# Performance work log

Hardware: AMD Instinct MI355X
Metric: run time of the kernel (lower is better)

The kernel has to match this reference:

```python
import jax, jax.numpy as jnp
import numpy as np

N = 10000; E = 160000; NF = 5; EF = 3; H = 8; C = 128; HC = H * C; G = 16

def _glorot(key, shape):
    s = float(np.sqrt(6.0 / (shape[0] + shape[-1])))
    return jax.random.uniform(key, shape, minval=-s, maxval=s, dtype=jnp.float32)

def setup_inputs():
    key = jax.random.key(0)
    ks = jax.random.split(key, 32)
    inp = {}
    inp["x"] = jax.random.normal(ks[0], (N, NF), dtype=jnp.float32)
    inp["edge_index"] = jax.random.randint(ks[1], (2, E), 0, N, dtype=jnp.int32)
    inp["edge_attr"] = jax.random.normal(ks[2], (E, EF), dtype=jnp.float32)
    inp["batch"] = jnp.sort(jax.random.randint(ks[3], (N,), 0, G, dtype=jnp.int32))
    ins = [NF, HC, HC, HC]
    i = 4
    for l in range(4):
        inp[f"W{l+1}"] = _glorot(ks[i], (ins[l], HC)); i += 1
        inp[f"We{l+1}"] = _glorot(ks[i], (EF, HC)); i += 1
        inp[f"as{l+1}"] = _glorot(ks[i], (H, C)); i += 1
        inp[f"ad{l+1}"] = _glorot(ks[i], (H, C)); i += 1
        inp[f"ae{l+1}"] = _glorot(ks[i], (H, C)); i += 1
        inp[f"b{l+1}"] = jnp.zeros((HC if l < 3 else C,), jnp.float32)
    inp["lin_w"] = _glorot(ks[i], (C, 1)) * 2.0
    inp["lin_b"] = jnp.zeros((1,), jnp.float32)
    return inp

def _gat(x, src, dst, ea, W, We, a_s, a_d, a_e, bias, concat):
    # PyG GATConv with edge_dim, add_self_loops=True, fill_value='mean'
    n = x.shape[0]
    cnt = jax.ops.segment_sum(jnp.ones((src.shape[0],), x.dtype), dst, n)
    loop_attr = jax.ops.segment_sum(ea, dst, n) / jnp.maximum(cnt, 1.0)[:, None]
    sl = jnp.arange(n, dtype=src.dtype)
    src2 = jnp.concatenate([src, sl])
    dst2 = jnp.concatenate([dst, sl])
    ea2 = jnp.concatenate([ea, loop_attr], axis=0)
    xl = (x @ W).reshape(n, H, C)                       # [N,H,C]
    a_src = jnp.einsum("nhc,hc->nh", xl, a_s)
    a_dst = jnp.einsum("nhc,hc->nh", xl, a_d)
    el = (ea2 @ We).reshape(-1, H, C)                    # [E2,H,C]
    alpha = a_src[src2] + a_dst[dst2] + jnp.einsum("ehc,hc->eh", el, a_e)
    alpha = jax.nn.leaky_relu(alpha, 0.2)
    m = jax.ops.segment_max(alpha, dst2, n)
    m = jnp.where(jnp.isfinite(m), m, 0.0)
    ex = jnp.exp(alpha - m[dst2])
    den = jax.ops.segment_sum(ex, dst2, n)
    alpha = ex / (den[dst2] + 1e-16)                     # segment softmax over dst
    out = jax.ops.segment_sum(alpha[:, :, None] * xl[src2], dst2, n)  # [N,H,C]
    if concat:
        return out.reshape(n, HC) + bias
    return out.mean(axis=1) + bias

def reference(x, edge_index, edge_attr, batch,
              W1, We1, as1, ad1, ae1, b1,
              W2, We2, as2, ad2, ae2, b2,
              W3, We3, as3, ad3, ae3, b3,
              W4, We4, as4, ad4, ae4, b4,
              lin_w, lin_b):
    src, dst = edge_index[0], edge_index[1]
    h = jax.nn.elu(_gat(x, src, dst, edge_attr, W1, We1, as1, ad1, ae1, b1, True))
    h = jax.nn.elu(_gat(h, src, dst, edge_attr, W2, We2, as2, ad2, ae2, b2, True))
    h = jax.nn.elu(_gat(h, src, dst, edge_attr, W3, We3, as3, ad3, ae3, b3, True))
    h = jax.nn.elu(_gat(h, src, dst, edge_attr, W4, We4, as4, ad4, ae4, b4, False))
    cnt = jax.ops.segment_sum(jnp.ones((N,), h.dtype), batch, G)
    pooled = jax.ops.segment_sum(h, batch, G) / jnp.maximum(cnt, 1.0)[:, None]
    return (pooled @ lin_w + lin_b).squeeze(-1)
```

## Files before the change

kernel.cpp:

```cpp
#include <hip/hip_runtime.h>
#include <math.h>

#define Nn 10000
#define En 160000
#define NF 5
#define EF 3
#define Hh 8
#define Cc 128
#define HC 1024
#define Gg 16

#define Mpad 10112

typedef __attribute__((ext_vector_type(8))) _Float16 half8;
typedef __attribute__((ext_vector_type(4))) float f32x4;


__device__ __forceinline__ void gl_lds16(const void* g, void* l) {
    __builtin_amdgcn_global_load_lds((const __attribute__((address_space(1))) void*)g,
                                     (__attribute__((address_space(3))) void*)l, 16, 0, 0);
}

__device__ __forceinline__ float elu_f(float v) {
    return (v > 0.f) ? v : expm1f(v);
}


__global__ void deg_sum_k(const int* __restrict__ dst, int* __restrict__ cnt) {
    int e = blockIdx.x * 256 + threadIdx.x;
    if (e >= En) return;
    atomicAdd(&cnt[dst[e]], 1);
}

__global__ __launch_bounds__(1024) void scan_k(const int* __restrict__ cnt,
                                               int* __restrict__ rowptr,
                                               int* __restrict__ fillptr,
                                               const int* __restrict__ batch,
                                               int* __restrict__ gstart) {
    __shared__ int sh[1024];
    int tid = threadIdx.x;
    int base = tid * 10;
    int loc[10];
    int tsum = 0;
#pragma unroll
    for (int j = 0; j < 10; ++j) {
        int i = base + j;
        int v = (i < Nn) ? cnt[i] : 0;
        loc[j] = tsum;
        tsum += v;
    }
    sh[tid] = tsum;
    __syncthreads();
    for (int off = 1; off < 1024; off <<= 1) {
        int t = (tid >= off) ? sh[tid - off] : 0;
        __syncthreads();
        sh[tid] += t;
        __syncthreads();
    }
    int excl = sh[tid] - tsum;
#pragma unroll
    for (int j = 0; j < 10; ++j) {
        int i = base + j;
        if (i < Nn) {
            rowptr[i] = excl + loc[j];
            fillptr[i] = excl + loc[j];
        }
    }
    if (tid == 1023) rowptr[Nn] = sh[1023];
#pragma unroll
    for (int j = 0; j < 10; ++j) {
        int i = base + j;
        if (i < Nn) {
            int b = batch[i];
            if (i == 0) {
                for (int g = 0; g <= b; ++g) gstart[g] = 0;
            } else {
                int pb = batch[i - 1];
                for (int g = pb + 1; g <= b; ++g) gstart[g] = i;
            }
            if (i == Nn - 1) {
                for (int g = b + 1; g <= Gg; ++g) gstart[g] = Nn;
            }
        }
    }
}

__global__ void csr_fill_k(const int* __restrict__ src, const int* __restrict__ dst,
                           const float* __restrict__ ea, int* __restrict__ fillptr,
                           float4* __restrict__ eaP, float* __restrict__ loop_attr) {
    int e = blockIdx.x * 256 + threadIdx.x;
    if (e >= En) return;
    int d = dst[e];
    float e0 = ea[e * 3 + 0], e1 = ea[e * 3 + 1], e2 = ea[e * 3 + 2];
    int pos = atomicAdd(&fillptr[d], 1);
    eaP[pos] = make_float4(e0, e1, e2, __int_as_float(src[e]));
    atomicAdd(&loop_attr[d * 3 + 0], e0);
    atomicAdd(&loop_attr[d * 3 + 1], e1);
    atomicAdd(&loop_attr[d * 3 + 2], e2);
}


__global__ void wae_all_k(const float* __restrict__ We1, const float* __restrict__ ae1,
                          const float* __restrict__ We2, const float* __restrict__ ae2,
                          const float* __restrict__ We3, const float* __restrict__ ae3,
                          const float* __restrict__ We4, const float* __restrict__ ae4,
                          float* __restrict__ w_ae_all) {
    int t = threadIdx.x;
    if (t >= 96) return;
    int l = t / 24, idx = t % 24;
    int f = idx >> 3, h = idx & 7;
    const float* We = (l == 0) ? We1 : (l == 1) ? We2 : (l == 2) ? We3 : We4;
    const float* ae = (l == 0) ? ae1 : (l == 1) ? ae2 : (l == 2) ? ae3 : ae4;
    float s = 0.f;
    for (int c = 0; c < Cc; ++c) s += We[f * HC + h * Cc + c] * ae[h * Cc + c];
    w_ae_all[l * 24 + f * 8 + h] = s;
}

__global__ __launch_bounds__(1024) void wsplit_all_k(const float* __restrict__ W2,
                                                     const float* __restrict__ W3,
                                                     const float* __restrict__ W4,
                                                     _Float16* __restrict__ Wt16) {
    __shared__ float tile[32][33];
    int z = blockIdx.z;
    const float* W = (z == 0) ? W2 : (z == 1) ? W3 : W4;
    int nb = blockIdx.x * 32, kb = blockIdx.y * 32;
    tile[threadIdx.y][threadIdx.x] = W[(size_t)(kb + threadIdx.y) * HC + nb + threadIdx.x];
    __syncthreads();
    float x = tile[threadIdx.x][threadIdx.y];
    int n = nb + threadIdx.y, k = kb + threadIdx.x;
    Wt16[(size_t)z * HC * HC + (size_t)n * HC + k] = (_Float16)x;
}


__global__ void gemm_k5(const float* __restrict__ x, const float* __restrict__ Wm,
                        const float* __restrict__ a_s, const float* __restrict__ a_d,
                        _Float16* __restrict__ out16,
                        float* __restrict__ a_srcB, float* __restrict__ a_dstB) {
    int n = blockIdx.x;
    int tid = threadIdx.x;
    __shared__ float xr[8];
    __shared__ float vrow[HC];
    if (tid < NF) xr[tid] = x[n * NF + tid];
    __syncthreads();
    float x0 = xr[0], x1 = xr[1], x2 = xr[2], x3 = xr[3], x4 = xr[4];
    for (int j = tid; j < HC; j += 256) {
        float v = x0 * Wm[j] + x1 * Wm[HC + j] + x2 * Wm[2 * HC + j]
                + x3 * Wm[3 * HC + j] + x4 * Wm[4 * HC + j];
        out16[(size_t)n * HC + j] = (_Float16)v;
        vrow[j] = v;
    }
    __syncthreads();
    int w = tid >> 6, lane = tid & 63;
#pragma unroll
    for (int q = 0; q < 2; ++q) {
        int h = w * 2 + q;
        float v0 = vrow[h * Cc + lane], v1 = vrow[h * Cc + 64 + lane];
        float s1 = v0 * a_s[h * Cc + lane] + v1 * a_s[h * Cc + 64 + lane];
        float s2 = v0 * a_d[h * Cc + lane] + v1 * a_d[h * Cc + 64 + lane];
#pragma unroll
        for (int off = 32; off; off >>= 1) {
            s1 += __shfl_xor(s1, off);
            s2 += __shfl_xor(s2, off);
        }
        if (lane == 0) { a_srcB[n * 8 + h] = s1; a_dstB[n * 8 + h] = s2; }
    }
}

__global__ __launch_bounds__(256) void gemm_mfma(const _Float16* __restrict__ A,
                                                 const _Float16* __restrict__ Bt,
                                                 const float* __restrict__ a_s,
                                                 const float* __restrict__ a_d,
                                                 _Float16* __restrict__ C16,
                                                 float* __restrict__ a_srcB,
                                                 float* __restrict__ a_dstB) {
    __shared__ _Float16 As[128 * 32];
    __shared__ _Float16 Bs[128 * 32];
    __shared__ float ps[128][2];
    __shared__ float pd[128][2];
    int tid = threadIdx.x;
    int wave = tid >> 6, lane = tid & 63;
    int wr = wave >> 1, wc = wave & 1;
    int row0 = blockIdx.y * 128;
    int col0 = blockIdx.x * 128;
    int h = blockIdx.x;

    f32x4 acc[4][4];
#pragma unroll
    for (int i = 0; i < 4; ++i)
#pragma unroll
        for (int j = 0; j < 4; ++j) acc[i][j] = (f32x4){0.f, 0.f, 0.f, 0.f};

    int srow = lane >> 2;
    int scol = (lane & 3) * 8;
    int fr = lane & 15;
    int fk = (lane >> 4) * 8;

    for (int kb = 0; kb < 1024; kb += 32) {
#pragma unroll
        for (int cc = 0; cc < 2; ++cc) {
            int c = wave + cc * 4;
            int r = c * 16 + srow;
            gl_lds16(A + (size_t)(row0 + r) * 1024 + kb + scol, &As[c * 512 + lane * 8]);
            gl_lds16(Bt + (size_t)(col0 + r) * 1024 + kb + scol, &Bs[c * 512 + lane * 8]);
        }
        __syncthreads();

        half8 af[4], bf[4];
#pragma unroll
        for (int i = 0; i < 4; ++i)
            af[i] = *(const half8*)&As[(wr * 64 + i * 16 + fr) * 32 + fk];
#pragma unroll
        for (int j = 0; j < 4; ++j)
            bf[j] = *(const half8*)&Bs[(wc * 64 + j * 16 + fr) * 32 + fk];
#pragma unroll
        for (int i = 0; i < 4; ++i)
#pragma unroll
            for (int j = 0; j < 4; ++j)
                acc[i][j] = __builtin_amdgcn_mfma_f32_16x16x32_f16(af[i], bf[j], acc[i][j],
                                                                   0, 0, 0);
        __syncthreads();
    }

    int cn = lane & 15, rq = (lane >> 4) * 4;
#pragma unroll
    for (int i = 0; i < 4; ++i) {
        int rbase = row0 + wr * 64 + i * 16 + rq;
#pragma unroll
        for (int j = 0; j < 4; ++j) {
            int col = col0 + wc * 64 + j * 16 + cn;
#pragma unroll
            for (int r = 0; r < 4; ++r) {
                int row = rbase + r;
                if (row < Nn) C16[(size_t)row * HC + col] = (_Float16)acc[i][j][r];
            }
        }
    }
    float asv[4], adv[4];
#pragma unroll
    for (int j = 0; j < 4; ++j) {
        int c = wc * 64 + j * 16 + cn;
        asv[j] = a_s[h * Cc + c];
        adv[j] = a_d[h * Cc + c];
    }
#pragma unroll
    for (int i = 0; i < 4; ++i)
#pragma unroll
        for (int r = 0; r < 4; ++r) {
            float rs = acc[i][0][r] * asv[0] + acc[i][1][r] * asv[1]
                     + acc[i][2][r] * asv[2] + acc[i][3][r] * asv[3];
            float rd = acc[i][0][r] * adv[0] + acc[i][1][r] * adv[1]
                     + acc[i][2][r] * adv[2] + acc[i][3][r] * adv[3];
#pragma unroll
            for (int off = 1; off < 16; off <<= 1) {
                rs += __shfl_xor(rs, off);
                rd += __shfl_xor(rd, off);
            }
            if (cn == 0) {
                int rib = wr * 64 + i * 16 + rq + r;
                ps[rib][wc] = rs;
                pd[rib][wc] = rd;
            }
        }
    __syncthreads();
    if (tid < 128) {
        int row = row0 + tid;
        if (row < Nn) {
            a_srcB[row * 8 + h] = ps[tid][0] + ps[tid][1];
            a_dstB[row * 8 + h] = pd[tid][0] + pd[tid][1];
        }
    }
}


__global__ __launch_bounds__(256) void aggregate_k(const _Float16* __restrict__ xl16,
                                                   const float4* __restrict__ eaP,
                                                   const float* __restrict__ loop_attr,
                                                   const float* __restrict__ a_srcB,
                                                   const float* __restrict__ a_dstB,
                                                   const float* __restrict__ w_ae,
                                                   const int* __restrict__ rowptr,
                                                   const float* __restrict__ bias,
                                                   const float* __restrict__ lin_w,
                                                   _Float16* __restrict__ A2,
                                                   float* __restrict__ dnode,
                                                   int raw_mode) {
    __shared__ float cmbA[3][1024];
    __shared__ float cmbS[3][64];
    int sub = threadIdx.x >> 6;
    int lane = threadIdx.x & 63;
    int n = blockIdx.x;
    int beg = rowptr[n], end = rowptr[n + 1];
    int hc = lane >> 3;

    float w0c = w_ae[hc], w1c = w_ae[8 + hc], w2c = w_ae[16 + hc];
    float adst_n = a_dstB[n * 8 + hc];
    float asrc_n = a_srcB[n * 8 + hc];
    float invd = 1.0f / fmaxf((float)(end - beg), 1.0f);
    float f0 = loop_attr[n * 3 + 0] * invd;
    float f1 = loop_attr[n * 3 + 1] * invd;
    float f2 = loop_attr[n * 3 + 2] * invd;
    float av = asrc_n + adst_n + f0 * w0c + f1 * w1c + f2 * w2c;
    float aself = (av > 0.f) ? av : 0.2f * av;

    float acc[16];
    float s;
    int loff = lane * 16;
    if (sub == 0) {
        const _Float16* r = xl16 + (size_t)n * HC + loff;
        half8 r0 = *(const half8*)r;
        half8 r1 = *(const half8*)(r + 8);
#pragma unroll
        for (int j = 0; j < 8; ++j) {
            acc[j] = (float)r0[j];
            acc[8 + j] = (float)r1[j];
        }
        s = 1.0f;
    } else {
#pragma unroll
        for (int j = 0; j < 16; ++j) acc[j] = 0.f;
        s = 0.0f;
    }

    for (int i0 = beg + sub; i0 < end; i0 += 16) {
        bool v1 = (i0 + 4 < end), v2 = (i0 + 8 < end), v3 = (i0 + 12 < end);
        int i1 = v1 ? i0 + 4 : i0;
        int i2 = v2 ? i0 + 8 : i0;
        int i3 = v3 ? i0 + 12 : i0;
        float4 e0 = eaP[i0], e1 = eaP[i1], e2 = eaP[i2], e3 = eaP[i3];
        int s0 = __float_as_int(e0.w), s1 = __float_as_int(e1.w);
        int s2 = __float_as_int(e2.w), s3 = __float_as_int(e3.w);
        float as0 = a_srcB[s0 * 8 + hc], as1 = a_srcB[s1 * 8 + hc];
        float as2 = a_srcB[s2 * 8 + hc], as3 = a_srcB[s3 * 8 + hc];
        const _Float16* p0 = xl16 + (size_t)s0 * HC + loff;
        const _Float16* p1 = xl16 + (size_t)s1 * HC + loff;
        const _Float16* p2 = xl16 + (size_t)s2 * HC + loff;
        const _Float16* p3 = xl16 + (size_t)s3 * HC + loff;
        half8 q0a = *(const half8*)p0, q0b = *(const half8*)(p0 + 8);
        half8 q1a = *(const half8*)p1, q1b = *(const half8*)(p1 + 8);
        half8 q2a = *(const half8*)p2, q2b = *(const half8*)(p2 + 8);
        half8 q3a = *(const half8*)p3, q3b = *(const half8*)(p3 + 8);
        float al0 = as0 + adst_n + e0.x * w0c + e0.y * w1c + e0.z * w2c;
        float al1 = as1 + adst_n + e1.x * w0c + e1.y * w1c + e1.z * w2c;
        float al2 = as2 + adst_n + e2.x * w0c + e2.y * w1c + e2.z * w2c;
        float al3 = as3 + adst_n + e3.x * w0c + e3.y * w1c + e3.z * w2c;
        al0 = (al0 > 0.f) ? al0 : 0.2f * al0;
        al1 = (al1 > 0.f) ? al1 : 0.2f * al1;
        al2 = (al2 > 0.f) ? al2 : 0.2f * al2;
        al3 = (al3 > 0.f) ? al3 : 0.2f * al3;
        float u0 = __expf(al0 - aself);
        float u1 = v1 ? __expf(al1 - aself) : 0.f;
        float u2 = v2 ? __expf(al2 - aself) : 0.f;
        float u3 = v3 ? __expf(al3 - aself) : 0.f;
        s += u0 + u1 + u2 + u3;
#pragma unroll
        for (int j = 0; j < 8; ++j) {
            float t0 = acc[j], t1 = acc[8 + j];
            t0 = fmaf(u0, (float)q0a[j], t0);  t1 = fmaf(u0, (float)q0b[j], t1);
            t0 = fmaf(u1, (float)q1a[j], t0);  t1 = fmaf(u1, (float)q1b[j], t1);
            t0 = fmaf(u2, (float)q2a[j], t0);  t1 = fmaf(u2, (float)q2b[j], t1);
            t0 = fmaf(u3, (float)q3a[j], t0);  t1 = fmaf(u3, (float)q3b[j], t1);
            acc[j] = t0; acc[8 + j] = t1;
        }
    }

    if (sub != 0) {
#pragma unroll
        for (int j = 0; j < 4; ++j)
            *(float4*)&cmbA[sub - 1][loff + j * 4] = *(const float4*)&acc[j * 4];
        cmbS[sub - 1][lane] = s;
    }
    __syncthreads();
    if (sub != 0) return;

#pragma unroll
    for (int k = 0; k < 3; ++k) {
        s += cmbS[k][lane];
#pragma unroll
        for (int j = 0; j < 4; ++j) {
            float4 c4 = *(const float4*)&cmbA[k][loff + j * 4];
            acc[j * 4 + 0] += c4.x;
            acc[j * 4 + 1] += c4.y;
            acc[j * 4 + 2] += c4.z;
            acc[j * 4 + 3] += c4.w;
        }
    }
    float inv = 1.f / (s + 1e-16f);

    if (!raw_mode) {
        int ch = loff;
        half8 hv0, hv1;
#pragma unroll
        for (int j = 0; j < 8; ++j) {
            hv0[j] = (_Float16)elu_f(fmaf(acc[j], inv, bias[ch + j]));
            hv1[j] = (_Float16)elu_f(fmaf(acc[8 + j], inv, bias[ch + 8 + j]));
        }
        _Float16* p = A2 + (size_t)n * 1024 + ch;
        *(half8*)p = hv0;
        *(half8*)(p + 8) = hv1;
    } else {
#pragma unroll
        for (int j = 0; j < 16; ++j) acc[j] *= inv;
#pragma unroll
        for (int off = 8; off < 64; off <<= 1)
#pragma unroll
            for (int j = 0; j < 16; ++j) acc[j] += __shfl_xor(acc[j], off);
        int c0 = (lane & 7) * 16;
        float partial = 0.f;
#pragma unroll
        for (int j = 0; j < 16; ++j) {
            float v = elu_f(acc[j] * 0.125f + bias[c0 + j]);
            partial = fmaf(v, lin_w[c0 + j], partial);
        }
#pragma unroll
        for (int off = 1; off < 8; off <<= 1) partial += __shfl_xor(partial, off);
        if (lane == 0) dnode[n] = partial;
    }
}


__global__ __launch_bounds__(256) void pool_final_k(const float* __restrict__ dnode,
                                                    const int* __restrict__ gstart,
                                                    const float* __restrict__ lin_b,
                                                    float* __restrict__ out) {
    __shared__ float sh[256];
    int g = blockIdx.x;
    int tid = threadIdx.x;
    int s = gstart[g], e = gstart[g + 1];
    float acc = 0.f;
    for (int n = s + tid; n < e; n += 256) acc += dnode[n];
    sh[tid] = acc;
    __syncthreads();
    for (int off = 128; off; off >>= 1) {
        if (tid < off) sh[tid] += sh[tid + off];
        __syncthreads();
    }
    if (tid == 0) out[g] = sh[0] / fmaxf((float)(e - s), 1.f) + lin_b[0];
}


extern "C" void kernel_launch(void* const* d_in, const int* in_sizes, int n_in,
                              void* d_out, int out_size, void* d_ws, size_t ws_size,
                              hipStream_t stream) {
    const float* x = (const float*)d_in[0];
    const int* ei = (const int*)d_in[1];
    const float* ea = (const float*)d_in[2];
    const int* batch = (const int*)d_in[3];
    const float *Wl[4], *Wel[4], *asl[4], *adl[4], *ael[4], *bl[4];
    for (int l = 0; l < 4; ++l) {
        Wl[l] = (const float*)d_in[4 + 6 * l];
        Wel[l] = (const float*)d_in[5 + 6 * l];
        asl[l] = (const float*)d_in[6 + 6 * l];
        adl[l] = (const float*)d_in[7 + 6 * l];
        ael[l] = (const float*)d_in[8 + 6 * l];
        bl[l] = (const float*)d_in[9 + 6 * l];
    }
    const float* lin_w = (const float*)d_in[28];
    const float* lin_b = (const float*)d_in[29];
    const int* srcA = ei;
    const int* dstA = ei + En;

    float* Wp = (float*)d_ws;
    size_t o = 0;
    _Float16* A2 = (_Float16*)(Wp + o); o += (size_t)Mpad * 512;
    _Float16* Wt16 = (_Float16*)(Wp + o); o += (size_t)3 * HC * HC / 2;
    _Float16* xl16 = (_Float16*)(Wp + o); o += (size_t)Nn * HC / 2;
    float4* eaP = (float4*)(Wp + o); o += (size_t)En * 4;
    float* loop_attr = Wp + o; o += Nn * 3;
    int* cnt = (int*)(Wp + o); o += Nn;
    int* rowptr = (int*)(Wp + o); o += Nn + 1;
    int* fillptr = (int*)(Wp + o); o += Nn;
    int* gstart = (int*)(Wp + o); o += Gg + 1;
    float* a_srcB = Wp + o; o += Nn * Hh;
    float* a_dstB = Wp + o; o += Nn * Hh;
    float* w_ae_all = Wp + o; o += 128;
    float* dnode = Wp + o; o += Nn;

    hipMemsetAsync(cnt, 0, Nn * sizeof(int), stream);
    hipMemsetAsync(loop_attr, 0, Nn * 3 * sizeof(float), stream);

    deg_sum_k<<<(En + 255) / 256, 256, 0, stream>>>(dstA, cnt);
    scan_k<<<1, 1024, 0, stream>>>(cnt, rowptr, fillptr, batch, gstart);
    csr_fill_k<<<(En + 255) / 256, 256, 0, stream>>>(srcA, dstA, ea, fillptr, eaP,
                                                     loop_attr);
    wae_all_k<<<1, 128, 0, stream>>>(Wel[0], ael[0], Wel[1], ael[1], Wel[2], ael[2],
                                     Wel[3], ael[3], w_ae_all);
    wsplit_all_k<<<dim3(32, 32, 3), dim3(32, 32), 0, stream>>>(Wl[1], Wl[2], Wl[3], Wt16);

    for (int l = 0; l < 4; ++l) {
        if (l == 0)
            gemm_k5<<<Nn, 256, 0, stream>>>(x, Wl[0], asl[0], adl[0], xl16, a_srcB, a_dstB);
        else
            gemm_mfma<<<dim3(HC / 128, Mpad / 128), 256, 0, stream>>>(
                A2, Wt16 + (size_t)(l - 1) * HC * HC, asl[l], adl[l], xl16, a_srcB, a_dstB);
        aggregate_k<<<Nn, 256, 0, stream>>>(xl16, eaP, loop_attr, a_srcB,
                                            a_dstB, w_ae_all + l * 24, rowptr,
                                            bl[l], lin_w, A2, dnode,
                                            (l == 3) ? 1 : 0);
    }
    pool_final_k<<<Gg, 256, 0, stream>>>(dnode, gstart, lin_b, (float*)d_out);
}
```

Measured before the change: 556.5 us.

## Assign one wavefront per node in aggregation, removing LDS cross-wave combine

```diff
diff --git a/kernel.cpp b/kernel.cpp
--- a/kernel.cpp
+++ b/kernel.cpp
@@ -272,23 +272,21 @@
 }
 
 
-__global__ __launch_bounds__(256) void aggregate_k(const _Float16* __restrict__ xl16,
-                                                   const float4* __restrict__ eaP,
-                                                   const float* __restrict__ loop_attr,
-                                                   const float* __restrict__ a_srcB,
-                                                   const float* __restrict__ a_dstB,
-                                                   const float* __restrict__ w_ae,
-                                                   const int* __restrict__ rowptr,
-                                                   const float* __restrict__ bias,
-                                                   const float* __restrict__ lin_w,
-                                                   _Float16* __restrict__ A2,
-                                                   float* __restrict__ dnode,
-                                                   int raw_mode) {
-    __shared__ float cmbA[3][1024];
-    __shared__ float cmbS[3][64];
-    int sub = threadIdx.x >> 6;
+__global__ __launch_bounds__(256, 4) void aggregate_k(const _Float16* __restrict__ xl16,
+                                                      const float4* __restrict__ eaP,
+                                                      const float* __restrict__ loop_attr,
+                                                      const float* __restrict__ a_srcB,
+                                                      const float* __restrict__ a_dstB,
+                                                      const float* __restrict__ w_ae,
+                                                      const int* __restrict__ rowptr,
+                                                      const float* __restrict__ bias,
+                                                      const float* __restrict__ lin_w,
+                                                      _Float16* __restrict__ A2,
+                                                      float* __restrict__ dnode,
+                                                      int raw_mode) {
     int lane = threadIdx.x & 63;
-    int n = blockIdx.x;
+    int n = blockIdx.x * 4 + (threadIdx.x >> 6);
+    if (n >= Nn) return;
     int beg = rowptr[n], end = rowptr[n + 1];
     int hc = lane >> 3;
 
@@ -302,30 +300,24 @@
     float av = asrc_n + adst_n + f0 * w0c + f1 * w1c + f2 * w2c;
     float aself = (av > 0.f) ? av : 0.2f * av;
 
+    int loff = lane * 16;
+
+    const _Float16* rp = xl16 + (size_t)n * HC + loff;
+    half8 r0 = *(const half8*)rp;
+    half8 r1 = *(const half8*)(rp + 8);
     float acc[16];
-    float s;
-    int loff = lane * 16;
-    if (sub == 0) {
-        const _Float16* r = xl16 + (size_t)n * HC + loff;
-        half8 r0 = *(const half8*)r;
-        half8 r1 = *(const half8*)(r + 8);
-#pragma unroll
-        for (int j = 0; j < 8; ++j) {
-            acc[j] = (float)r0[j];
-            acc[8 + j] = (float)r1[j];
-        }
-        s = 1.0f;
-    } else {
-#pragma unroll
-        for (int j = 0; j < 16; ++j) acc[j] = 0.f;
-        s = 0.0f;
-    }
-
-    for (int i0 = beg + sub; i0 < end; i0 += 16) {
-        bool v1 = (i0 + 4 < end), v2 = (i0 + 8 < end), v3 = (i0 + 12 < end);
-        int i1 = v1 ? i0 + 4 : i0;
-        int i2 = v2 ? i0 + 8 : i0;
-        int i3 = v3 ? i0 + 12 : i0;
+#pragma unroll
+    for (int j = 0; j < 8; ++j) {
+        acc[j] = (float)r0[j];
+        acc[8 + j] = (float)r1[j];
+    }
+    float s = 1.0f;
+
+    for (int i0 = beg; i0 < end; i0 += 4) {
+        bool v1 = (i0 + 1 < end), v2 = (i0 + 2 < end), v3 = (i0 + 3 < end);
+        int i1 = v1 ? i0 + 1 : i0;
+        int i2 = v2 ? i0 + 2 : i0;
+        int i3 = v3 ? i0 + 3 : i0;
         float4 e0 = eaP[i0], e1 = eaP[i1], e2 = eaP[i2], e3 = eaP[i3];
         int s0 = __float_as_int(e0.w), s1 = __float_as_int(e1.w);
         int s2 = __float_as_int(e2.w), s3 = __float_as_int(e3.w);
@@ -363,27 +355,6 @@
         }
     }
 
-    if (sub != 0) {
-#pragma unroll
-        for (int j = 0; j < 4; ++j)
-            *(float4*)&cmbA[sub - 1][loff + j * 4] = *(const float4*)&acc[j * 4];
-        cmbS[sub - 1][lane] = s;
-    }
-    __syncthreads();
-    if (sub != 0) return;
-
-#pragma unroll
-    for (int k = 0; k < 3; ++k) {
-        s += cmbS[k][lane];
-#pragma unroll
-        for (int j = 0; j < 4; ++j) {
-            float4 c4 = *(const float4*)&cmbA[k][loff + j * 4];
-            acc[j * 4 + 0] += c4.x;
-            acc[j * 4 + 1] += c4.y;
-            acc[j * 4 + 2] += c4.z;
-            acc[j * 4 + 3] += c4.w;
-        }
-    }
     float inv = 1.f / (s + 1e-16f);
 
     if (!raw_mode) {
@@ -492,10 +463,10 @@
         else
             gemm_mfma<<<dim3(HC / 128, Mpad / 128), 256, 0, stream>>>(
                 A2, Wt16 + (size_t)(l - 1) * HC * HC, asl[l], adl[l], xl16, a_srcB, a_dstB);
-        aggregate_k<<<Nn, 256, 0, stream>>>(xl16, eaP, loop_attr, a_srcB,
-                                            a_dstB, w_ae_all + l * 24, rowptr,
-                                            bl[l], lin_w, A2, dnode,
-                                            (l == 3) ? 1 : 0);
+        aggregate_k<<<(Nn + 3) / 4, 256, 0, stream>>>(xl16, eaP, loop_attr, a_srcB,
+                                                      a_dstB, w_ae_all + l * 24, rowptr,
+                                                      bl[l], lin_w, A2, dnode,
+                                                      (l == 3) ? 1 : 0);
     }
     pool_final_k<<<Gg, 256, 0, stream>>>(dnode, gstart, lin_b, (float*)d_out);
 }
```

New measurement: 572.0 us. 1.03x slower.
